# Kernel optimization log

Hardware: AMD Instinct MI355X
Metric: run time of the kernel (lower is better)

Reference implementation:

```python
import jax, jax.numpy as jnp
import numpy as np

N_NODES = 50000
N_EDGES = 800000
F_IN = 256          # hidden_dims[-1]
DIMS = [256, 128, 32]  # output_dim chain from source
ZK = 8              # z_dim // 2
K_SAMPLES = 8


def _glorot(key, shape):
    fan_in, fan_out = shape
    lim = np.sqrt(6.0 / (fan_in + fan_out)).astype(np.float32)
    return jax.random.uniform(key, shape, jnp.float32, -lim, lim)


def setup_inputs() -> dict:
    key = jax.random.key(0)
    ks = jax.random.split(key, 8)
    x = jax.random.normal(ks[0], (N_NODES, F_IN), jnp.float32)
    edge_index = jax.random.randint(ks[1], (2, N_EDGES), 0, N_NODES, jnp.int64)
    W1 = _glorot(ks[2], (F_IN, DIMS[0]));  b1 = jnp.zeros((DIMS[0],), jnp.float32)
    W2 = _glorot(ks[3], (DIMS[0], DIMS[1])); b2 = jnp.zeros((DIMS[1],), jnp.float32)
    W3 = _glorot(ks[4], (DIMS[1], DIMS[2])); b3 = jnp.zeros((DIMS[2],), jnp.float32)
    Wk = _glorot(ks[5], (DIMS[2], ZK));      bk = jnp.zeros((ZK,), jnp.float32)
    return {"x": x, "edge_index": edge_index, "K": K_SAMPLES,
            "W1": W1, "b1": b1, "W2": W2, "b2": b2,
            "W3": W3, "b3": b3, "Wk": Wk, "bk": bk}


def _gcn_conv(x, W, b, src, dst, norm, n):
    # PyG GCNConv: h = X W; out[i] = sum_{j->i} norm_ji * h[j] + b (self loops included in src/dst)
    h = x @ W
    msg = h[src] * norm[:, None]
    return jax.ops.segment_sum(msg, dst, num_segments=n) + b


def reference(x, edge_index, K, W1, b1, W2, b2, W3, b3, Wk, bk):
    n = x.shape[0]
    loops = jnp.arange(n, dtype=edge_index.dtype)
    src = jnp.concatenate([edge_index[0], loops])
    dst = jnp.concatenate([edge_index[1], loops])
    deg = jax.ops.segment_sum(jnp.ones_like(src, dtype=x.dtype), dst, num_segments=n)
    dinv = jax.lax.rsqrt(jnp.maximum(deg, 1.0))  # deg >= 1 with self loops
    norm = dinv[src] * dinv[dst]

    # GCNNModel: stacked GraphConvolution layers with ReLU (eval mode -> dropout is identity)
    h = jax.nn.relu(_gcn_conv(x, W1, b1, src, dst, norm, n))
    h = jax.nn.relu(_gcn_conv(h, W2, b2, src, dst, norm, n))
    h = jax.nn.relu(_gcn_conv(h, W3, b3, src, dst, norm, n))

    # K-sample branch: x tiled to [N, K, D], GraphConvolutionK applies shared conv per slice
    hk = jnp.broadcast_to(h[:, None, :], (n, K, h.shape[-1]))
    zk = jax.vmap(lambda xi: jax.nn.relu(_gcn_conv(xi, Wk, bk, src, dst, norm, n)),
                  in_axes=1, out_axes=1)(hk)  # [N, K, ZK]

    # InnerProductDecoder over original edge_index for each of the K samples -> [K, E]
    s, d = edge_index[0], edge_index[1]
    logits = jnp.einsum('ekd,ekd->ke', zk[s], zk[d])
    return logits
```

## Files before the change

### kernel.cpp

```cpp
#include <hip/hip_runtime.h>
#include <hip/hip_bf16.h>

#define THREADS 256

typedef __attribute__((ext_vector_type(2))) float f32x2;
typedef __attribute__((ext_vector_type(4))) float f32x4;
typedef __attribute__((ext_vector_type(8))) float f32x8;
typedef __attribute__((ext_vector_type(8))) short short8;
typedef __attribute__((ext_vector_type(4))) unsigned short u16x4;
typedef __attribute__((ext_vector_type(8))) unsigned short u16x8;

__device__ inline unsigned short f2bf(float f) {
    unsigned int u = __builtin_bit_cast(unsigned int, f);
    unsigned int r = (u + 0x7FFFu + ((u >> 16) & 1u)) >> 16;
    return (unsigned short)r;
}
__device__ inline float bf2f(unsigned short h) {
    unsigned int u = ((unsigned int)h) << 16;
    return __builtin_bit_cast(float, u);
}
__device__ __forceinline__ f32x8 bfv8(u16x8 v) {
    f32x8 r;
#pragma unroll
    for (int j = 0; j < 8; ++j) r[j] = bf2f(v[j]);
    return r;
}
__device__ __forceinline__ f32x4 bfv4(u16x4 v) {
    f32x4 r;
#pragma unroll
    for (int j = 0; j < 4; ++j) r[j] = bf2f(v[j]);
    return r;
}


__global__ __launch_bounds__(256) void init_cnt_kernel(int* cnt, int n) {
    int i = blockIdx.x * blockDim.x + threadIdx.x;
    if (i < n) cnt[i] = 1;
}

__global__ __launch_bounds__(256) void count_edges_kernel(const int* ei, int* cnt, int E) {
    int e = blockIdx.x * blockDim.x + threadIdx.x;
    if (e < E) atomicAdd(&cnt[ei[E + e]], 1);
}

__global__ __launch_bounds__(256) void scan_p1_kernel(const int* __restrict__ cnt,
                                                      int* __restrict__ bsum, int n) {
    __shared__ int sh[256];
    int i = blockIdx.x * 256 + threadIdx.x;
    int v = (i < n) ? cnt[i] : 0;
    sh[threadIdx.x] = v;
    __syncthreads();
#pragma unroll
    for (int off = 128; off > 0; off >>= 1) {
        if ((int)threadIdx.x < off) sh[threadIdx.x] += sh[threadIdx.x + off];
        __syncthreads();
    }
    if (threadIdx.x == 0) bsum[blockIdx.x] = sh[0];
}

__global__ __launch_bounds__(1024) void scan_p2_kernel(int* __restrict__ bsum, int nb) {
    __shared__ int sh[1024];
    int v = ((int)threadIdx.x < nb) ? bsum[threadIdx.x] : 0;
    sh[threadIdx.x] = v;
    __syncthreads();
    for (int off = 1; off < 1024; off <<= 1) {
        int t = (threadIdx.x >= (unsigned)off) ? sh[threadIdx.x - off] : 0;
        __syncthreads();
        sh[threadIdx.x] += t;
        __syncthreads();
    }
    if ((int)threadIdx.x < nb) bsum[threadIdx.x] = sh[threadIdx.x] - v;
}

__global__ __launch_bounds__(256) void scan_p3_kernel(const int* __restrict__ cnt,
                                                      const int* __restrict__ bsum,
                                                      int* __restrict__ row_ptr, int n) {
    __shared__ int sh[256];
    int i = blockIdx.x * 256 + threadIdx.x;
    int v = (i < n) ? cnt[i] : 0;
    sh[threadIdx.x] = v;
    __syncthreads();
    for (int off = 1; off < 256; off <<= 1) {
        int t = (threadIdx.x >= (unsigned)off) ? sh[threadIdx.x - off] : 0;
        __syncthreads();
        sh[threadIdx.x] += t;
        __syncthreads();
    }
    int excl = sh[threadIdx.x] - v + bsum[blockIdx.x];
    if (i < n) row_ptr[i] = excl;
    if (i == n - 1) row_ptr[n] = excl + v;
}

__global__ __launch_bounds__(256) void prep_fused_kernel(const int* cnt, const int* row_ptr,
                                                         int* cursor, float* dinv,
                                                         int* src_sorted, int n) {
    int i = blockIdx.x * blockDim.x + threadIdx.x;
    if (i < n) {
        dinv[i] = rsqrtf((float)cnt[i]);
        int p = row_ptr[i];
        src_sorted[p] = i;
        cursor[i] = p + 1;
    }
}

__global__ __launch_bounds__(256) void fill_edges_kernel(const int* ei, int* cursor, int* src_sorted, int E) {
    int e = blockIdx.x * blockDim.x + threadIdx.x;
    if (e < E) {
        int s = ei[e];
        int d = ei[E + e];
        int pos = atomicAdd(&cursor[d], 1);
        src_sorted[pos] = s;
    }
}

__global__ __launch_bounds__(256) void convert_x_pack_kernel(const float* __restrict__ x,
                                                             unsigned short* __restrict__ Ap,
                                                             int n, int F) {
    long idx = (long)blockIdx.x * 256 + threadIdx.x;
    if (idx >= (long)n * 64) return;
    int row = (int)(idx >> 6), c = (int)(idx & 63);
    int kg = c >> 2, ks = c & 3;
    bool ishi = kg < 8;
    int klocal = (kg & 7) * 32 + ks * 8;
    const float* src = &x[(long)row * F + klocal];
    f32x4 v0 = *(const f32x4*)src;
    f32x4 v1 = *(const f32x4*)(src + 4);
    u16x8 o;
#pragma unroll
    for (int j = 0; j < 4; ++j) {
        unsigned short h0 = f2bf(v0[j]);
        unsigned short h1 = f2bf(v1[j]);
        o[j]     = ishi ? h0 : f2bf(v0[j] - bf2f(h0));
        o[j + 4] = ishi ? h1 : f2bf(v1[j] - bf2f(h1));
    }
    size_t chunk = (size_t)(row >> 4) * 1024 + (size_t)kg * 64 + (row & 15) * 4 + ks;
    *(u16x8*)&Ap[chunk * 8] = o;
}

__global__ __launch_bounds__(256) void convert_w_hi_kernel(const float* __restrict__ W,
                                                           unsigned short* __restrict__ Bp,
                                                           int K, int N) {
    int cpc = K / 8;
    int idx = blockIdx.x * 256 + threadIdx.x;
    if (idx >= N * cpc) return;
    int n = idx / cpc, ck = idx % cpc;
    int c = ck * 8;
    u16x8 o;
#pragma unroll
    for (int j = 0; j < 8; ++j) o[j] = f2bf(W[(long)(c + j) * N + n]);
    size_t chunk = ((size_t)(n >> 4) * (K / 32) + (ck >> 2)) * 64 + (ck & 3) * 16 + (n & 15);
    *(u16x8*)&Bp[chunk * 8] = o;
}

template <int BN>
__global__ __launch_bounds__(256) void gemm_pack_kernel(const unsigned short* __restrict__ Ap,
                                                        const unsigned short* __restrict__ Bp,
                                                        const float* __restrict__ dinv,
                                                        unsigned short* __restrict__ C,
                                                        int M, int N) {
    constexpr int NI = BN / 32;
    const int tid = threadIdx.x;
    const int wave = tid >> 6, l = tid & 63;
    const int wm = wave & 1, wn = wave >> 1;
    const int lr = l & 15, lg = l >> 4;
    const int rt0 = blockIdx.x * 4 + wm * 2;
    const int ct0 = wn * NI;
    const short8* ab = (const short8*)Ap + (size_t)rt0 * 1024 + lr * 4 + lg;
    const short8* bb = (const short8*)Bp + (size_t)ct0 * 512 + l;
    f32x4 acc[2][NI] = {};
#pragma unroll
    for (int kgb = 0; kgb < 8; ++kgb) {
        short8 b[NI], ah[2], al[2];
#pragma unroll
        for (int ni = 0; ni < NI; ++ni)
            b[ni] = bb[((size_t)ni * 8 + kgb) * 64];
#pragma unroll
        for (int i = 0; i < 2; ++i) {
            ah[i] = ab[((size_t)i * 16 + kgb) * 64];
            al[i] = ab[((size_t)i * 16 + 8 + kgb) * 64];
        }
#pragma unroll
        for (int i = 0; i < 2; ++i)
#pragma unroll
            for (int ni = 0; ni < NI; ++ni)
                acc[i][ni] = __builtin_amdgcn_mfma_f32_16x16x32_bf16(ah[i], b[ni], acc[i][ni], 0, 0, 0);
#pragma unroll
        for (int i = 0; i < 2; ++i)
#pragma unroll
            for (int ni = 0; ni < NI; ++ni)
                acc[i][ni] = __builtin_amdgcn_mfma_f32_16x16x32_bf16(al[i], b[ni], acc[i][ni], 0, 0, 0);
    }
#pragma unroll
    for (int i = 0; i < 2; ++i) {
        int rbase = blockIdx.x * 64 + (wm * 2 + i) * 16 + lg * 4;
#pragma unroll
        for (int ni = 0; ni < NI; ++ni) {
            int col = wn * (BN / 2) + ni * 16 + lr;
#pragma unroll
            for (int r = 0; r < 4; ++r) {
                int row = rbase + r;
                if (row < M) C[(long)row * N + col] = f2bf(acc[i][ni][r] * dinv[row]);
            }
        }
    }
}

template <int R4>
__device__ __forceinline__ f32x4 gather_sum_bf4(const u16x4* __restrict__ base,
                                                const int* __restrict__ src,
                                                int beg, int end) {
    f32x4 acc = {0.f, 0.f, 0.f, 0.f};
    int e = beg;
    for (; e + 16 <= end; e += 16) {
        u16x4 v[16];
#pragma unroll
        for (int j = 0; j < 16; ++j) v[j] = base[(long)src[e + j] * R4];
        f32x4 s0 = (bfv4(v[0]) + bfv4(v[1])) + (bfv4(v[2]) + bfv4(v[3]));
        f32x4 s1 = (bfv4(v[4]) + bfv4(v[5])) + (bfv4(v[6]) + bfv4(v[7]));
        f32x4 s2 = (bfv4(v[8]) + bfv4(v[9])) + (bfv4(v[10]) + bfv4(v[11]));
        f32x4 s3 = (bfv4(v[12]) + bfv4(v[13])) + (bfv4(v[14]) + bfv4(v[15]));
        acc += (s0 + s1) + (s2 + s3);
    }
    for (; e + 4 <= end; e += 4) {
        u16x4 v0 = base[(long)src[e] * R4],     v1 = base[(long)src[e + 1] * R4];
        u16x4 v2 = base[(long)src[e + 2] * R4], v3 = base[(long)src[e + 3] * R4];
        acc += (bfv4(v0) + bfv4(v1)) + (bfv4(v2) + bfv4(v3));
    }
    for (; e < end; ++e) acc += bfv4(base[(long)src[e] * R4]);
    return acc;
}

template <int R8>
__device__ __forceinline__ f32x8 gather_sum_bf(const u16x8* __restrict__ base,
                                               const int* __restrict__ src,
                                               int beg, int end) {
    f32x8 acc = {0.f, 0.f, 0.f, 0.f, 0.f, 0.f, 0.f, 0.f};
    int e = beg;
    for (; e + 8 <= end; e += 8) {
        u16x8 v0 = base[(long)src[e] * R8],     v1 = base[(long)src[e + 1] * R8];
        u16x8 v2 = base[(long)src[e + 2] * R8], v3 = base[(long)src[e + 3] * R8];
        u16x8 v4 = base[(long)src[e + 4] * R8], v5 = base[(long)src[e + 5] * R8];
        u16x8 v6 = base[(long)src[e + 6] * R8], v7 = base[(long)src[e + 7] * R8];
        acc += ((bfv8(v0) + bfv8(v1)) + (bfv8(v2) + bfv8(v3)))
             + ((bfv8(v4) + bfv8(v5)) + (bfv8(v6) + bfv8(v7)));
    }
    for (; e < end; ++e) acc += bfv8(base[(long)src[e] * R8]);
    return acc;
}

template <int G>
__device__ __forceinline__ f32x4 gather_sum(const f32x4* __restrict__ tsv,
                                            const int* __restrict__ src,
                                            int beg, int end, int lane) {
    f32x4 acc = {0.f, 0.f, 0.f, 0.f};
    int e = beg;
    for (; e + 8 <= end; e += 8) {
        int s0 = src[e], s1 = src[e + 1], s2 = src[e + 2], s3 = src[e + 3];
        int s4 = src[e + 4], s5 = src[e + 5], s6 = src[e + 6], s7 = src[e + 7];
        f32x4 v0 = tsv[(long)s0 * G + lane], v1 = tsv[(long)s1 * G + lane];
        f32x4 v2 = tsv[(long)s2 * G + lane], v3 = tsv[(long)s3 * G + lane];
        f32x4 v4 = tsv[(long)s4 * G + lane], v5 = tsv[(long)s5 * G + lane];
        f32x4 v6 = tsv[(long)s6 * G + lane], v7 = tsv[(long)s7 * G + lane];
        acc += ((v0 + v1) + (v2 + v3)) + ((v4 + v5) + (v6 + v7));
    }
    for (; e + 2 <= end; e += 2) {
        int s0 = src[e], s1 = src[e + 1];
        acc += tsv[(long)s0 * G + lane] + tsv[(long)s1 * G + lane];
    }
    if (e < end) acc += tsv[(long)src[e] * G + lane];
    return acc;
}

__global__ __launch_bounds__(256) void agg_split256_kernel(const unsigned short* __restrict__ ts,
                                                           const int* __restrict__ row_ptr,
                                                           const int* __restrict__ src_sorted,
                                                           const float* __restrict__ dinv,
                                                           const float* __restrict__ bias,
                                                           unsigned short* __restrict__ out_p,
                                                           int n) {
    int w = threadIdx.x >> 6, l = threadIdx.x & 63;
    int node = blockIdx.x * 4 + w;
    if (node >= n) return;
    const u16x4* base = (const u16x4*)ts + l;
    f32x4 acc = gather_sum_bf4<64>(base, src_sorted, row_ptr[node], row_ptr[node + 1]);
    float di = dinv[node];
    f32x4 b4 = *(const f32x4*)&bias[l * 4];
    f32x4 v = acc * di + b4;
    u16x4 hi, lo;
#pragma unroll
    for (int j = 0; j < 4; ++j) {
        float r = fmaxf(v[j], 0.f);
        hi[j] = f2bf(r);
        lo[j] = f2bf(r - bf2f(hi[j]));
    }
    int row = node & 15;
    int kg = l >> 3, ks = (l >> 1) & 3, half = l & 1;
    size_t choff = (size_t)(node >> 4) * 1024 + (size_t)kg * 64 + row * 4 + ks;
    *(u16x4*)&out_p[choff * 8 + half * 4] = hi;
    *(u16x4*)&out_p[(choff + 8 * 64) * 8 + half * 4] = lo;
}

__global__ __launch_bounds__(256) void agg_fused_w3_kernel(const unsigned short* __restrict__ ts,
                                                           const int* __restrict__ row_ptr,
                                                           const int* __restrict__ src_sorted,
                                                           const float* __restrict__ dinv,
                                                           const float* __restrict__ bias,
                                                           const float* __restrict__ W3,
                                                           float* __restrict__ ts3, int n) {
    __shared__ float W3s[128 * 32];
    __shared__ float hbuf[16][132];
    for (int i = threadIdx.x; i < 128 * 32; i += 256) W3s[i] = W3[i];
    __syncthreads();
    int g = threadIdx.x >> 4, lane = threadIdx.x & 15;
    int node = blockIdx.x * 16 + g;
    if (node >= n) return;
    const u16x8* base = (const u16x8*)ts + lane;
    f32x8 acc = gather_sum_bf<16>(base, src_sorted, row_ptr[node], row_ptr[node + 1]);
    float di = dinv[node];
    f32x8 b8 = *(const f32x8*)&bias[lane * 8];
    f32x8 v = acc * di + b8;
#pragma unroll
    for (int j = 0; j < 8; ++j) v[j] = fmaxf(v[j], 0.f);
    f32x4 vlo = {v[0], v[1], v[2], v[3]};
    f32x4 vhi = {v[4], v[5], v[6], v[7]};
    *(f32x4*)&hbuf[g][lane * 8] = vlo;
    *(f32x4*)&hbuf[g][lane * 8 + 4] = vhi;
    int c0 = lane * 2;
    float aj0 = 0.f, aj1 = 0.f;
#pragma unroll
    for (int k = 0; k < 128; k += 4) {
        f32x4 hv = *(const f32x4*)&hbuf[g][k];
        aj0 += hv[0] * W3s[k * 32 + c0] + hv[1] * W3s[(k + 1) * 32 + c0]
             + hv[2] * W3s[(k + 2) * 32 + c0] + hv[3] * W3s[(k + 3) * 32 + c0];
        aj1 += hv[0] * W3s[k * 32 + c0 + 1] + hv[1] * W3s[(k + 1) * 32 + c0 + 1]
             + hv[2] * W3s[(k + 2) * 32 + c0 + 1] + hv[3] * W3s[(k + 3) * 32 + c0 + 1];
    }
    f32x2 o = {aj0 * di, aj1 * di};
    *(f32x2*)&ts3[(long)node * 32 + c0] = o;
}

__global__ __launch_bounds__(256) void agg_fused_wk_kernel(const float* __restrict__ ts,
                                                           const int* __restrict__ row_ptr,
                                                           const int* __restrict__ src_sorted,
                                                           const float* __restrict__ dinv,
                                                           const float* __restrict__ bias,
                                                           const float* __restrict__ Wk,
                                                           float* __restrict__ tsk, int n) {
    __shared__ float Wks[32 * 8];
    __shared__ float hbuf[32][36];
    for (int i = threadIdx.x; i < 32 * 8; i += 256) Wks[i] = Wk[i];
    __syncthreads();
    int g = threadIdx.x >> 3, lane = threadIdx.x & 7;
    int node = blockIdx.x * 32 + g;
    if (node >= n) return;
    f32x4 acc = gather_sum<8>((const f32x4*)ts, src_sorted, row_ptr[node], row_ptr[node + 1], lane);
    float di = dinv[node];
    f32x4 b4 = *(const f32x4*)&bias[lane * 4];
    f32x4 v = acc * di + b4;
#pragma unroll
    for (int j = 0; j < 4; ++j) v[j] = fmaxf(v[j], 0.f);
    *(f32x4*)&hbuf[g][lane * 4] = v;
    float aj = 0.f;
#pragma unroll
    for (int k = 0; k < 32; k += 4) {
        f32x4 hv = *(const f32x4*)&hbuf[g][k];
        aj += hv[0] * Wks[k * 8 + lane] + hv[1] * Wks[(k + 1) * 8 + lane]
            + hv[2] * Wks[(k + 2) * 8 + lane] + hv[3] * Wks[(k + 3) * 8 + lane];
    }
    tsk[(long)node * 8 + lane] = aj * di;
}

__global__ __launch_bounds__(256) void agg_plain8_kernel(const float* __restrict__ ts,
                                                         const int* __restrict__ row_ptr,
                                                         const int* __restrict__ src_sorted,
                                                         const float* __restrict__ dinv,
                                                         const float* __restrict__ bias,
                                                         float* __restrict__ z, int n) {
    int g = threadIdx.x >> 1, lane = threadIdx.x & 1;
    int node = blockIdx.x * 128 + g;
    if (node >= n) return;
    f32x4 acc = gather_sum<2>((const f32x4*)ts, src_sorted, row_ptr[node], row_ptr[node + 1], lane);
    float di = dinv[node];
    f32x4 b4 = *(const f32x4*)&bias[lane * 4];
    f32x4 v = acc * di + b4;
#pragma unroll
    for (int j = 0; j < 4; ++j) v[j] = fmaxf(v[j], 0.f);
    *(f32x4*)&z[(long)node * 8 + lane * 4] = v;
}

__global__ __launch_bounds__(256) void decoder_kernel(const float* __restrict__ z,
                                                      const int* __restrict__ ei,
                                                      float* __restrict__ out,
                                                      int E, int K) {
    int e = blockIdx.x * blockDim.x + threadIdx.x;
    if (e >= E) return;
    int s = ei[e];
    int d = ei[E + e];
    const f32x4* zv = (const f32x4*)z;
    f32x4 a0 = zv[(long)s * 2], a1 = zv[(long)s * 2 + 1];
    f32x4 b0 = zv[(long)d * 2], b1 = zv[(long)d * 2 + 1];
    f32x4 p = a0 * b0 + a1 * b1;
    float acc = p[0] + p[1] + p[2] + p[3];
    for (int k = 0; k < K; k++) out[(long)k * E + e] = acc;
}


extern "C" void kernel_launch(void* const* d_in, const int* in_sizes, int n_in,
                              void* d_out, int out_size, void* d_ws, size_t ws_size,
                              hipStream_t stream) {
    const float* x  = (const float*)d_in[0];
    const int*   ei = (const int*)d_in[1];
    const float* W1 = (const float*)d_in[3];
    const float* b1 = (const float*)d_in[4];
    const float* W2 = (const float*)d_in[5];
    const float* b2 = (const float*)d_in[6];
    const float* W3 = (const float*)d_in[7];
    const float* b3 = (const float*)d_in[8];
    const float* Wk = (const float*)d_in[9];
    const float* bk = (const float*)d_in[10];
    float* out = (float*)d_out;

    const int D1 = in_sizes[4];
    const int D2 = in_sizes[6];
    const int F  = in_sizes[3] / D1;
    const int N  = in_sizes[0] / F;
    const int E  = in_sizes[1] / 2;
    const int K  = out_size / E;
    const int M  = E + N;
    const int Mpad = (N + 127) & ~127;

    size_t off = 0;
    auto alloc = [&](size_t bytes) -> void* {
        off = (off + 255) & ~(size_t)255;
        void* p = (char*)d_ws + off;
        off += bytes;
        return p;
    };
    int*   cnt        = (int*)alloc((size_t)N * sizeof(int));
    int*   row_ptr    = (int*)alloc((size_t)(N + 1) * sizeof(int));
    int*   cursor     = (int*)alloc((size_t)N * sizeof(int));
    int*   bsum       = (int*)alloc(1024 * sizeof(int));
    float* dinv       = (float*)alloc((size_t)N * sizeof(float));
    int*   src_sorted = (int*)alloc((size_t)M * sizeof(int));
    unsigned short* region_x = (unsigned short*)alloc((size_t)Mpad * 2 * F * sizeof(short));
    float* region_t   = (float*)alloc((size_t)Mpad * 256 * sizeof(float));
    unsigned short* Wt1 = (unsigned short*)alloc((size_t)D1 * F * sizeof(short));
    unsigned short* Wt2 = (unsigned short*)alloc((size_t)D2 * D1 * sizeof(short));
    float* ts3        = (float*)alloc((size_t)Mpad * 32 * sizeof(float));
    float* tsk        = (float*)alloc((size_t)Mpad * 8 * sizeof(float));
    float* z          = (float*)alloc((size_t)Mpad * 8 * sizeof(float));
    (void)ws_size; (void)n_in;

    unsigned short* xs  = region_x;
    unsigned short* h1s = region_x;
    unsigned short* ts1 = (unsigned short*)region_t;
    unsigned short* ts2 = (unsigned short*)region_t;

    int nbN = (N + THREADS - 1) / THREADS;
    int nbE = (E + THREADS - 1) / THREADS;

    init_cnt_kernel<<<nbN, THREADS, 0, stream>>>(cnt, N);
    count_edges_kernel<<<nbE, THREADS, 0, stream>>>(ei, cnt, E);
    scan_p1_kernel<<<nbN, THREADS, 0, stream>>>(cnt, bsum, N);
    scan_p2_kernel<<<1, 1024, 0, stream>>>(bsum, nbN);
    scan_p3_kernel<<<nbN, THREADS, 0, stream>>>(cnt, bsum, row_ptr, N);
    prep_fused_kernel<<<nbN, THREADS, 0, stream>>>(cnt, row_ptr, cursor, dinv, src_sorted, N);
    fill_edges_kernel<<<nbE, THREADS, 0, stream>>>(ei, cursor, src_sorted, E);

    convert_x_pack_kernel<<<(int)(((long)N * 64 + 255) / 256), THREADS, 0, stream>>>(x, xs, N, F);
    convert_w_hi_kernel<<<(D1 * (F / 8) + 255) / 256, THREADS, 0, stream>>>(W1, Wt1, F, D1);
    convert_w_hi_kernel<<<(D2 * (D1 / 8) + 255) / 256, THREADS, 0, stream>>>(W2, Wt2, D1, D2);

    gemm_pack_kernel<256><<<Mpad / 64, THREADS, 0, stream>>>(xs, Wt1, dinv, ts1, N, D1);
    agg_split256_kernel<<<(N + 3) / 4, THREADS, 0, stream>>>(ts1, row_ptr, src_sorted, dinv, b1, h1s, N);

    gemm_pack_kernel<128><<<Mpad / 64, THREADS, 0, stream>>>(h1s, Wt2, dinv, ts2, N, D2);
    agg_fused_w3_kernel<<<(N + 15) / 16, THREADS, 0, stream>>>(ts2, row_ptr, src_sorted, dinv, b2, W3, ts3, N);

    agg_fused_wk_kernel<<<(N + 31) / 32, THREADS, 0, stream>>>(ts3, row_ptr, src_sorted, dinv, b3, Wk, tsk, N);
    agg_plain8_kernel<<<(N + 127) / 128, THREADS, 0, stream>>>(tsk, row_ptr, src_sorted, dinv, bk, z, N);

    decoder_kernel<<<nbE, THREADS, 0, stream>>>(z, ei, out, E, K);
}
```

Measured before the change: 324.5 us.

## Merge independent preprocessing kernels via block-range dispatch and retune layer-2 aggregation

```diff
diff --git a/kernel.cpp b/kernel.cpp
--- a/kernel.cpp
+++ b/kernel.cpp
@@ -33,14 +33,123 @@
 }
 
 
-__global__ __launch_bounds__(256) void init_cnt_kernel(int* cnt, int n) {
-    int i = blockIdx.x * blockDim.x + threadIdx.x;
-    if (i < n) cnt[i] = 1;
-}
-
-__global__ __launch_bounds__(256) void count_edges_kernel(const int* ei, int* cnt, int E) {
-    int e = blockIdx.x * blockDim.x + threadIdx.x;
-    if (e < E) atomicAdd(&cnt[ei[E + e]], 1);
+__device__ __forceinline__ void convert_w_body(const float* __restrict__ W,
+                                               unsigned short* __restrict__ Bp,
+                                               int K, int N, int idx) {
+    int cpc = K / 8;
+    if (idx >= N * cpc) return;
+    int n = idx / cpc, ck = idx % cpc;
+    int c = ck * 8;
+    u16x8 o;
+#pragma unroll
+    for (int j = 0; j < 8; ++j) o[j] = f2bf(W[(long)(c + j) * N + n]);
+    size_t chunk = ((size_t)(n >> 4) * (K / 32) + (ck >> 2)) * 64 + (ck & 3) * 16 + (n & 15);
+    *(u16x8*)&Bp[chunk * 8] = o;
+}
+
+__device__ __forceinline__ void convert_x_body(const float* __restrict__ x,
+                                               unsigned short* __restrict__ Ap,
+                                               int n, int F, long idx) {
+    if (idx >= (long)n * 64) return;
+    int row = (int)(idx >> 6), c = (int)(idx & 63);
+    int kg = c >> 2, ks = c & 3;
+    bool ishi = kg < 8;
+    int klocal = (kg & 7) * 32 + ks * 8;
+    const float* src = &x[(long)row * F + klocal];
+    f32x4 v0 = *(const f32x4*)src;
+    f32x4 v1 = *(const f32x4*)(src + 4);
+    u16x8 o;
+#pragma unroll
+    for (int j = 0; j < 4; ++j) {
+        unsigned short h0 = f2bf(v0[j]);
+        unsigned short h1 = f2bf(v1[j]);
+        o[j]     = ishi ? h0 : f2bf(v0[j] - bf2f(h0));
+        o[j + 4] = ishi ? h1 : f2bf(v1[j] - bf2f(h1));
+    }
+    size_t chunk = (size_t)(row >> 4) * 1024 + (size_t)kg * 64 + (row & 15) * 4 + ks;
+    *(u16x8*)&Ap[chunk * 8] = o;
+}
+
+template <int BN>
+__device__ __forceinline__ void gemm_pack_body(const unsigned short* __restrict__ Ap,
+                                               const unsigned short* __restrict__ Bp,
+                                               const float* __restrict__ dinv,
+                                               unsigned short* __restrict__ C,
+                                               int M, int N, int bid) {
+    constexpr int NI = BN / 32;
+    const int tid = threadIdx.x;
+    const int wave = tid >> 6, l = tid & 63;
+    const int wm = wave & 1, wn = wave >> 1;
+    const int lr = l & 15, lg = l >> 4;
+    const int rt0 = bid * 4 + wm * 2;
+    const int ct0 = wn * NI;
+    const short8* ab = (const short8*)Ap + (size_t)rt0 * 1024 + lr * 4 + lg;
+    const short8* bb = (const short8*)Bp + (size_t)ct0 * 512 + l;
+    f32x4 acc[2][NI] = {};
+#pragma unroll
+    for (int kgb = 0; kgb < 8; ++kgb) {
+        short8 b[NI], ah[2], al[2];
+#pragma unroll
+        for (int ni = 0; ni < NI; ++ni)
+            b[ni] = bb[((size_t)ni * 8 + kgb) * 64];
+#pragma unroll
+        for (int i = 0; i < 2; ++i) {
+            ah[i] = ab[((size_t)i * 16 + kgb) * 64];
+            al[i] = ab[((size_t)i * 16 + 8 + kgb) * 64];
+        }
+#pragma unroll
+        for (int i = 0; i < 2; ++i)
+#pragma unroll
+            for (int ni = 0; ni < NI; ++ni)
+                acc[i][ni] = __builtin_amdgcn_mfma_f32_16x16x32_bf16(ah[i], b[ni], acc[i][ni], 0, 0, 0);
+#pragma unroll
+        for (int i = 0; i < 2; ++i)
+#pragma unroll
+            for (int ni = 0; ni < NI; ++ni)
+                acc[i][ni] = __builtin_amdgcn_mfma_f32_16x16x32_bf16(al[i], b[ni], acc[i][ni], 0, 0, 0);
+    }
+#pragma unroll
+    for (int i = 0; i < 2; ++i) {
+        int rbase = bid * 64 + (wm * 2 + i) * 16 + lg * 4;
+#pragma unroll
+        for (int ni = 0; ni < NI; ++ni) {
+            int col = wn * (BN / 2) + ni * 16 + lr;
+#pragma unroll
+            for (int r = 0; r < 4; ++r) {
+                int row = rbase + r;
+                if (row < M) C[(long)row * N + col] = f2bf(acc[i][ni][r] * dinv[row]);
+            }
+        }
+    }
+}
+
+
+__global__ __launch_bounds__(256) void k1_init_convw_kernel(int* cnt, int n, int nbI,
+                                                            const float* W1, unsigned short* Wt1,
+                                                            int F, int D1, int nbW1,
+                                                            const float* W2, unsigned short* Wt2,
+                                                            int D1b, int D2) {
+    int b = blockIdx.x;
+    if (b < nbI) {
+        int i = b * 256 + threadIdx.x;
+        if (i < n) cnt[i] = 1;
+    } else if (b < nbI + nbW1) {
+        convert_w_body(W1, Wt1, F, D1, (b - nbI) * 256 + threadIdx.x);
+    } else {
+        convert_w_body(W2, Wt2, D1b, D2, (b - nbI - nbW1) * 256 + threadIdx.x);
+    }
+}
+
+__global__ __launch_bounds__(256) void k2_count_convx_kernel(const int* ei, int* cnt, int E, int nbC,
+                                                             const float* x, unsigned short* Ap,
+                                                             int n, int F) {
+    int b = blockIdx.x;
+    if (b < nbC) {
+        int e = b * 256 + threadIdx.x;
+        if (e < E) atomicAdd(&cnt[ei[E + e]], 1);
+    } else {
+        convert_x_body(x, Ap, n, F, (long)(b - nbC) * 256 + threadIdx.x);
+    }
 }
 
 __global__ __launch_bounds__(256) void scan_p1_kernel(const int* __restrict__ cnt,
@@ -72,9 +181,12 @@
     if ((int)threadIdx.x < nb) bsum[threadIdx.x] = sh[threadIdx.x] - v;
 }
 
-__global__ __launch_bounds__(256) void scan_p3_kernel(const int* __restrict__ cnt,
-                                                      const int* __restrict__ bsum,
-                                                      int* __restrict__ row_ptr, int n) {
+__global__ __launch_bounds__(256) void scan_p3_prep_kernel(const int* __restrict__ cnt,
+                                                           const int* __restrict__ bsum,
+                                                           int* __restrict__ row_ptr,
+                                                           float* __restrict__ dinv,
+                                                           int* __restrict__ cursor,
+                                                           int* __restrict__ src_sorted, int n) {
     __shared__ int sh[256];
     int i = blockIdx.x * 256 + threadIdx.x;
     int v = (i < n) ? cnt[i] : 0;
@@ -87,69 +199,34 @@
         __syncthreads();
     }
     int excl = sh[threadIdx.x] - v + bsum[blockIdx.x];
-    if (i < n) row_ptr[i] = excl;
+    if (i < n) {
+        row_ptr[i] = excl;
+        dinv[i] = rsqrtf((float)v);
+        src_sorted[excl] = i;
+        cursor[i] = excl + 1;
+    }
     if (i == n - 1) row_ptr[n] = excl + v;
 }
 
-__global__ __launch_bounds__(256) void prep_fused_kernel(const int* cnt, const int* row_ptr,
-                                                         int* cursor, float* dinv,
-                                                         int* src_sorted, int n) {
-    int i = blockIdx.x * blockDim.x + threadIdx.x;
-    if (i < n) {
-        dinv[i] = rsqrtf((float)cnt[i]);
-        int p = row_ptr[i];
-        src_sorted[p] = i;
-        cursor[i] = p + 1;
-    }
-}
-
-__global__ __launch_bounds__(256) void fill_edges_kernel(const int* ei, int* cursor, int* src_sorted, int E) {
-    int e = blockIdx.x * blockDim.x + threadIdx.x;
-    if (e < E) {
-        int s = ei[e];
-        int d = ei[E + e];
-        int pos = atomicAdd(&cursor[d], 1);
-        src_sorted[pos] = s;
-    }
-}
-
-__global__ __launch_bounds__(256) void convert_x_pack_kernel(const float* __restrict__ x,
-                                                             unsigned short* __restrict__ Ap,
-                                                             int n, int F) {
-    long idx = (long)blockIdx.x * 256 + threadIdx.x;
-    if (idx >= (long)n * 64) return;
-    int row = (int)(idx >> 6), c = (int)(idx & 63);
-    int kg = c >> 2, ks = c & 3;
-    bool ishi = kg < 8;
-    int klocal = (kg & 7) * 32 + ks * 8;
-    const float* src = &x[(long)row * F + klocal];
-    f32x4 v0 = *(const f32x4*)src;
-    f32x4 v1 = *(const f32x4*)(src + 4);
-    u16x8 o;
-#pragma unroll
-    for (int j = 0; j < 4; ++j) {
-        unsigned short h0 = f2bf(v0[j]);
-        unsigned short h1 = f2bf(v1[j]);
-        o[j]     = ishi ? h0 : f2bf(v0[j] - bf2f(h0));
-        o[j + 4] = ishi ? h1 : f2bf(v1[j] - bf2f(h1));
-    }
-    size_t chunk = (size_t)(row >> 4) * 1024 + (size_t)kg * 64 + (row & 15) * 4 + ks;
-    *(u16x8*)&Ap[chunk * 8] = o;
-}
-
-__global__ __launch_bounds__(256) void convert_w_hi_kernel(const float* __restrict__ W,
-                                                           unsigned short* __restrict__ Bp,
-                                                           int K, int N) {
-    int cpc = K / 8;
-    int idx = blockIdx.x * 256 + threadIdx.x;
-    if (idx >= N * cpc) return;
-    int n = idx / cpc, ck = idx % cpc;
-    int c = ck * 8;
-    u16x8 o;
-#pragma unroll
-    for (int j = 0; j < 8; ++j) o[j] = f2bf(W[(long)(c + j) * N + n]);
-    size_t chunk = ((size_t)(n >> 4) * (K / 32) + (ck >> 2)) * 64 + (ck & 3) * 16 + (n & 15);
-    *(u16x8*)&Bp[chunk * 8] = o;
+__global__ __launch_bounds__(256) void k6_gemm_fill_kernel(const unsigned short* __restrict__ Ap,
+                                                           const unsigned short* __restrict__ Bp,
+                                                           const float* __restrict__ dinv,
+                                                           unsigned short* __restrict__ C,
+                                                           int M, int N, int nbG,
+                                                           const int* __restrict__ ei,
+                                                           int* __restrict__ cursor,
+                                                           int* __restrict__ src_sorted, int E) {
+    if ((int)blockIdx.x < nbG) {
+        gemm_pack_body<256>(Ap, Bp, dinv, C, M, N, blockIdx.x);
+    } else {
+        int e = (blockIdx.x - nbG) * 256 + threadIdx.x;
+        if (e < E) {
+            int s = ei[e];
+            int d = ei[E + e];
+            int pos = atomicAdd(&cursor[d], 1);
+            src_sorted[pos] = s;
+        }
+    }
 }
 
 template <int BN>
@@ -158,51 +235,7 @@
                                                         const float* __restrict__ dinv,
                                                         unsigned short* __restrict__ C,
                                                         int M, int N) {
-    constexpr int NI = BN / 32;
-    const int tid = threadIdx.x;
-    const int wave = tid >> 6, l = tid & 63;
-    const int wm = wave & 1, wn = wave >> 1;
-    const int lr = l & 15, lg = l >> 4;
-    const int rt0 = blockIdx.x * 4 + wm * 2;
-    const int ct0 = wn * NI;
-    const short8* ab = (const short8*)Ap + (size_t)rt0 * 1024 + lr * 4 + lg;
-    const short8* bb = (const short8*)Bp + (size_t)ct0 * 512 + l;
-    f32x4 acc[2][NI] = {};
-#pragma unroll
-    for (int kgb = 0; kgb < 8; ++kgb) {
-        short8 b[NI], ah[2], al[2];
-#pragma unroll
-        for (int ni = 0; ni < NI; ++ni)
-            b[ni] = bb[((size_t)ni * 8 + kgb) * 64];
-#pragma unroll
-        for (int i = 0; i < 2; ++i) {
-            ah[i] = ab[((size_t)i * 16 + kgb) * 64];
-            al[i] = ab[((size_t)i * 16 + 8 + kgb) * 64];
-        }
-#pragma unroll
-        for (int i = 0; i < 2; ++i)
-#pragma unroll
-            for (int ni = 0; ni < NI; ++ni)
-                acc[i][ni] = __builtin_amdgcn_mfma_f32_16x16x32_bf16(ah[i], b[ni], acc[i][ni], 0, 0, 0);
-#pragma unroll
-        for (int i = 0; i < 2; ++i)
-#pragma unroll
-            for (int ni = 0; ni < NI; ++ni)
-                acc[i][ni] = __builtin_amdgcn_mfma_f32_16x16x32_bf16(al[i], b[ni], acc[i][ni], 0, 0, 0);
-    }
-#pragma unroll
-    for (int i = 0; i < 2; ++i) {
-        int rbase = blockIdx.x * 64 + (wm * 2 + i) * 16 + lg * 4;
-#pragma unroll
-        for (int ni = 0; ni < NI; ++ni) {
-            int col = wn * (BN / 2) + ni * 16 + lr;
-#pragma unroll
-            for (int r = 0; r < 4; ++r) {
-                int row = rbase + r;
-                if (row < M) C[(long)row * N + col] = f2bf(acc[i][ni][r] * dinv[row]);
-            }
-        }
-    }
+    gemm_pack_body<BN>(Ap, Bp, dinv, C, M, N, blockIdx.x);
 }
 
 template <int R4>
@@ -227,24 +260,6 @@
         acc += (bfv4(v0) + bfv4(v1)) + (bfv4(v2) + bfv4(v3));
     }
     for (; e < end; ++e) acc += bfv4(base[(long)src[e] * R4]);
-    return acc;
-}
-
-template <int R8>
-__device__ __forceinline__ f32x8 gather_sum_bf(const u16x8* __restrict__ base,
-                                               const int* __restrict__ src,
-                                               int beg, int end) {
-    f32x8 acc = {0.f, 0.f, 0.f, 0.f, 0.f, 0.f, 0.f, 0.f};
-    int e = beg;
-    for (; e + 8 <= end; e += 8) {
-        u16x8 v0 = base[(long)src[e] * R8],     v1 = base[(long)src[e + 1] * R8];
-        u16x8 v2 = base[(long)src[e + 2] * R8], v3 = base[(long)src[e + 3] * R8];
-        u16x8 v4 = base[(long)src[e + 4] * R8], v5 = base[(long)src[e + 5] * R8];
-        u16x8 v6 = base[(long)src[e + 6] * R8], v7 = base[(long)src[e + 7] * R8];
-        acc += ((bfv8(v0) + bfv8(v1)) + (bfv8(v2) + bfv8(v3)))
-             + ((bfv8(v4) + bfv8(v5)) + (bfv8(v6) + bfv8(v7)));
-    }
-    for (; e < end; ++e) acc += bfv8(base[(long)src[e] * R8]);
     return acc;
 }
 
@@ -308,35 +323,28 @@
                                                            const float* __restrict__ W3,
                                                            float* __restrict__ ts3, int n) {
     __shared__ float W3s[128 * 32];
-    __shared__ float hbuf[16][132];
+    __shared__ float hbuf[8][132];
     for (int i = threadIdx.x; i < 128 * 32; i += 256) W3s[i] = W3[i];
     __syncthreads();
-    int g = threadIdx.x >> 4, lane = threadIdx.x & 15;
-    int node = blockIdx.x * 16 + g;
+    int g = threadIdx.x >> 5, lane = threadIdx.x & 31;
+    int node = blockIdx.x * 8 + g;
     if (node >= n) return;
-    const u16x8* base = (const u16x8*)ts + lane;
-    f32x8 acc = gather_sum_bf<16>(base, src_sorted, row_ptr[node], row_ptr[node + 1]);
+    const u16x4* base = (const u16x4*)ts + lane;
+    f32x4 acc = gather_sum_bf4<32>(base, src_sorted, row_ptr[node], row_ptr[node + 1]);
     float di = dinv[node];
-    f32x8 b8 = *(const f32x8*)&bias[lane * 8];
-    f32x8 v = acc * di + b8;
-#pragma unroll
-    for (int j = 0; j < 8; ++j) v[j] = fmaxf(v[j], 0.f);
-    f32x4 vlo = {v[0], v[1], v[2], v[3]};
-    f32x4 vhi = {v[4], v[5], v[6], v[7]};
-    *(f32x4*)&hbuf[g][lane * 8] = vlo;
-    *(f32x4*)&hbuf[g][lane * 8 + 4] = vhi;
-    int c0 = lane * 2;
-    float aj0 = 0.f, aj1 = 0.f;
+    f32x4 b4 = *(const f32x4*)&bias[lane * 4];
+    f32x4 v = acc * di + b4;
+#pragma unroll
+    for (int j = 0; j < 4; ++j) v[j] = fmaxf(v[j], 0.f);
+    *(f32x4*)&hbuf[g][lane * 4] = v;
+    float aj = 0.f;
 #pragma unroll
     for (int k = 0; k < 128; k += 4) {
         f32x4 hv = *(const f32x4*)&hbuf[g][k];
-        aj0 += hv[0] * W3s[k * 32 + c0] + hv[1] * W3s[(k + 1) * 32 + c0]
-             + hv[2] * W3s[(k + 2) * 32 + c0] + hv[3] * W3s[(k + 3) * 32 + c0];
-        aj1 += hv[0] * W3s[k * 32 + c0 + 1] + hv[1] * W3s[(k + 1) * 32 + c0 + 1]
-             + hv[2] * W3s[(k + 2) * 32 + c0 + 1] + hv[3] * W3s[(k + 3) * 32 + c0 + 1];
-    }
-    f32x2 o = {aj0 * di, aj1 * di};
-    *(f32x2*)&ts3[(long)node * 32 + c0] = o;
+        aj += hv[0] * W3s[k * 32 + lane] + hv[1] * W3s[(k + 1) * 32 + lane]
+            + hv[2] * W3s[(k + 2) * 32 + lane] + hv[3] * W3s[(k + 3) * 32 + lane];
+    }
+    ts3[(long)node * 32 + lane] = aj * di;
 }
 
 __global__ __launch_bounds__(256) void agg_fused_wk_kernel(const float* __restrict__ ts,
@@ -456,29 +464,25 @@
     unsigned short* ts1 = (unsigned short*)region_t;
     unsigned short* ts2 = (unsigned short*)region_t;
 
-    int nbN = (N + THREADS - 1) / THREADS;
-    int nbE = (E + THREADS - 1) / THREADS;
-
-    init_cnt_kernel<<<nbN, THREADS, 0, stream>>>(cnt, N);
-    count_edges_kernel<<<nbE, THREADS, 0, stream>>>(ei, cnt, E);
+    const int nbN = (N + THREADS - 1) / THREADS;
+    const int nbE = (E + THREADS - 1) / THREADS;
+    const int nbX = (int)(((long)N * 64 + 255) / 256);
+    const int nbW1 = (D1 * (F / 8) + 255) / 256;
+    const int nbW2 = (D2 * (D1 / 8) + 255) / 256;
+    const int nbG1 = Mpad / 64;
+
+    k1_init_convw_kernel<<<nbN + nbW1 + nbW2, THREADS, 0, stream>>>(
+        cnt, N, nbN, W1, Wt1, F, D1, nbW1, W2, Wt2, D1, D2);
+    k2_count_convx_kernel<<<nbE + nbX, THREADS, 0, stream>>>(ei, cnt, E, nbE, x, xs, N, F);
     scan_p1_kernel<<<nbN, THREADS, 0, stream>>>(cnt, bsum, N);
     scan_p2_kernel<<<1, 1024, 0, stream>>>(bsum, nbN);
-    scan_p3_kernel<<<nbN, THREADS, 0, stream>>>(cnt, bsum, row_ptr, N);
-    prep_fused_kernel<<<nbN, THREADS, 0, stream>>>(cnt, row_ptr, cursor, dinv, src_sorted, N);
-    fill_edges_kernel<<<nbE, THREADS, 0, stream>>>(ei, cursor, src_sorted, E);
-
-    convert_x_pack_kernel<<<(int)(((long)N * 64 + 255) / 256), THREADS, 0, stream>>>(x, xs, N, F);
-    convert_w_hi_kernel<<<(D1 * (F / 8) + 255) / 256, THREADS, 0, stream>>>(W1, Wt1, F, D1);
-    convert_w_hi_kernel<<<(D2 * (D1 / 8) + 255) / 256, THREADS, 0, stream>>>(W2, Wt2, D1, D2);
-
-    gemm_pack_kernel<256><<<Mpad / 64, THREADS, 0, stream>>>(xs, Wt1, dinv, ts1, N, D1);
+    scan_p3_prep_kernel<<<nbN, THREADS, 0, stream>>>(cnt, bsum, row_ptr, dinv, cursor, src_sorted, N);
+    k6_gemm_fill_kernel<<<nbG1 + nbE, THREADS, 0, stream>>>(
+        xs, Wt1, dinv, ts1, N, D1, nbG1, ei, cursor, src_sorted, E);
     agg_split256_kernel<<<(N + 3) / 4, THREADS, 0, stream>>>(ts1, row_ptr, src_sorted, dinv, b1, h1s, N);
-
-    gemm_pack_kernel<128><<<Mpad / 64, THREADS, 0, stream>>>(h1s, Wt2, dinv, ts2, N, D2);
-    agg_fused_w3_kernel<<<(N + 15) / 16, THREADS, 0, stream>>>(ts2, row_ptr, src_sorted, dinv, b2, W3, ts3, N);
-
+    gemm_pack_kernel<128><<<nbG1, THREADS, 0, stream>>>(h1s, Wt2, dinv, ts2, N, D2);
+    agg_fused_w3_kernel<<<(N + 7) / 8, THREADS, 0, stream>>>(ts2, row_ptr, src_sorted, dinv, b2, W3, ts3, N);
     agg_fused_wk_kernel<<<(N + 31) / 32, THREADS, 0, stream>>>(ts3, row_ptr, src_sorted, dinv, b3, Wk, tsk, N);
     agg_plain8_kernel<<<(N + 127) / 128, THREADS, 0, stream>>>(tsk, row_ptr, src_sorted, dinv, bk, z, N);
-
     decoder_kernel<<<nbE, THREADS, 0, stream>>>(z, ei, out, E, K);
 }
```

Result: no change. 318.7 us (-1.8%).
